# Kernel optimization log

Measured on AMD Instinct MI355X. Metric: run time of the kernel, lower is better.

Reference implementation:

```python
import jax, jax.numpy as jnp
import numpy as np

B, S, DIM, H, DH, DEPTH, NCLS = 4, 2048, 128, 8, 128, 2, 10
M = 128          # number of FAVOR+ random features
CHUNK = 128      # chunk size for causal linear attention
INNER = H * DH   # performer-pytorch: dim_head=dim -> inner_dim = heads*dim
FF = 4 * DIM


def layernorm(x, g, b, eps=1e-5):
    mu = jnp.mean(x, axis=-1, keepdims=True)
    var = jnp.mean((x - mu) ** 2, axis=-1, keepdims=True)
    return (x - mu) * jax.lax.rsqrt(var + eps) * g + b


def softmax_kernel(data, proj, is_query, eps=1e-4):
    # FAVOR+ positive softmax-kernel features. data: [B,H,S,DH], proj: [M,DH]
    norm = DH ** -0.25
    ratio = M ** -0.5
    d = data * norm
    dd = jnp.einsum('bhsd,md->bhsm', d, proj)
    diag = 0.5 * jnp.sum(d * d, axis=-1, keepdims=True)
    if is_query:
        stab = jnp.max(dd, axis=-1, keepdims=True)
    else:
        stab = jnp.max(dd, axis=(-2, -1), keepdims=True)
    stab = jax.lax.stop_gradient(stab)
    return ratio * (jnp.exp(dd - diag - stab) + eps)


def causal_linear_attention(qp, kp, v):
    # qp,kp: [B,H,S,M], v: [B,H,S,DH]; chunked prefix-sum causal linear attention
    b, h, s, m = qp.shape
    d = v.shape[-1]
    nc = s // CHUNK
    def to_chunks(t):
        return t.reshape(b, h, nc, CHUNK, -1).transpose(2, 0, 1, 3, 4)
    qc, kc, vc = to_chunks(qp), to_chunks(kp), to_chunks(v)
    tri = jnp.tril(jnp.ones((CHUNK, CHUNK), qp.dtype))
    def step(carry, inp):
        kv_sum, k_sum = carry           # [b,h,m,d], [b,h,m]
        qi, ki, vi = inp                # [b,h,CHUNK,*]
        attn = jnp.einsum('bhim,bhjm->bhij', qi, ki) * tri
        num = jnp.einsum('bhij,bhjd->bhid', attn, vi) \
            + jnp.einsum('bhim,bhmd->bhid', qi, kv_sum)
        den = jnp.sum(attn, axis=-1) + jnp.einsum('bhim,bhm->bhi', qi, k_sum)
        out = num / (den[..., None] + 1e-6)
        kv_sum = kv_sum + jnp.einsum('bhjm,bhjd->bhmd', ki, vi)
        k_sum = k_sum + jnp.sum(ki, axis=2)
        return (kv_sum, k_sum), out
    init = (jnp.zeros((b, h, m, d), qp.dtype), jnp.zeros((b, h, m), qp.dtype))
    _, out = jax.lax.scan(step, init, (qc, kc, vc))
    return out.transpose(1, 2, 0, 3, 4).reshape(b, h, s, d)


def setup_inputs():
    key = jax.random.key(0)
    ks = jax.random.split(key, 12)
    rng = np.random.default_rng(0)
    # sinusoidal positional encoding [S, DIM]
    pe = np.zeros((S, DIM), np.float32)
    pos = np.arange(S)[:, None].astype(np.float32)
    div = np.exp(np.arange(0, DIM, 2).astype(np.float32) * (-np.log(10000.0) / DIM))
    pe[:, 0::2] = np.sin(pos * div)
    pe[:, 1::2] = np.cos(pos * div)
    # orthogonal random feature projections per layer [DEPTH, M, DH]
    proj = np.stack([
        (np.linalg.qr(rng.standard_normal((DH, DH)))[0][:M] * np.sqrt(DH))
        for _ in range(DEPTH)
    ]).astype(np.float32)
    def gn(k, shape, scale):
        return jax.random.normal(k, shape, jnp.float32) * scale
    return {
        'x': gn(ks[0], (B, S, 1), 1.0),
        'lin_w': gn(ks[1], (1, DIM), 1.0),
        'lin_b': jnp.zeros((DIM,), jnp.float32),
        'pe': jnp.asarray(pe),
        'proj': jnp.asarray(proj),
        'ln1_g': jnp.ones((DEPTH, DIM), jnp.float32),
        'ln1_b': jnp.zeros((DEPTH, DIM), jnp.float32),
        'wq': gn(ks[2], (DEPTH, DIM, INNER), DIM ** -0.5),
        'wk': gn(ks[3], (DEPTH, DIM, INNER), DIM ** -0.5),
        'wv': gn(ks[4], (DEPTH, DIM, INNER), DIM ** -0.5),
        'wo': gn(ks[5], (DEPTH, INNER, DIM), INNER ** -0.5),
        'wo_b': jnp.zeros((DEPTH, DIM), jnp.float32),
        'ln2_g': jnp.ones((DEPTH, DIM), jnp.float32),
        'ln2_b': jnp.zeros((DEPTH, DIM), jnp.float32),
        'ff1_w': gn(ks[6], (DEPTH, DIM, FF), DIM ** -0.5),
        'ff1_b': jnp.zeros((DEPTH, FF), jnp.float32),
        'ff2_w': gn(ks[7], (DEPTH, FF, DIM), FF ** -0.5),
        'ff2_b': jnp.zeros((DEPTH, DIM), jnp.float32),
        'fin_w': gn(ks[8], (DIM, NCLS), DIM ** -0.5),
        'fin_b': jnp.zeros((NCLS,), jnp.float32),
    }


def reference(x, lin_w, lin_b, pe, proj, ln1_g, ln1_b, wq, wk, wv, wo, wo_b,
              ln2_g, ln2_b, ff1_w, ff1_b, ff2_w, ff2_b, fin_w, fin_b):
    h = x @ lin_w + lin_b            # [B,S,DIM]
    h = h + pe[None]
    for l in range(DEPTH):
        # --- pre-norm FAVOR+ causal self-attention ---
        y = layernorm(h, ln1_g[l], ln1_b[l])
        def split(t):  # [B,S,INNER] -> [B,H,S,DH]
            return t.reshape(B, S, H, DH).transpose(0, 2, 1, 3)
        q, k, v = split(y @ wq[l]), split(y @ wk[l]), split(y @ wv[l])
        qp = softmax_kernel(q, proj[l], True)
        kp = softmax_kernel(k, proj[l], False)
        o = causal_linear_attention(qp, kp, v)          # [B,H,S,DH]
        o = o.transpose(0, 2, 1, 3).reshape(B, S, INNER)
        h = h + (o @ wo[l] + wo_b[l])
        # --- pre-norm FFN ---
        y = layernorm(h, ln2_g[l], ln2_b[l])
        f = jax.nn.gelu(y @ ff1_w[l] + ff1_b[l]) @ ff2_w[l] + ff2_b[l]
        h = h + f
    pooled = jnp.mean(h, axis=1)     # [B,DIM]
    return pooled @ fin_w + fin_b    # [B,NCLS]
```

## Files before the change

kernel.cpp:

```cpp
#include <hip/hip_runtime.h>
#include <hip/hip_bf16.h>

#define Bb 4
#define Ss 2048
#define DIMc 128
#define Hh 8
#define DHc 128
#define Mf 128
#define CH 128
#define NCc 16
#define INNERc 1024
#define FFc 512

union F4 { float4 v; float f[4]; };
typedef unsigned short u16;

typedef __bf16 bf16x8 __attribute__((ext_vector_type(8)));
typedef float  f32x4  __attribute__((ext_vector_type(4)));

__device__ __forceinline__ unsigned fkey(float f){
  unsigned b = __float_as_uint(f);
  return (b & 0x80000000u) ? ~b : (b | 0x80000000u);
}
__device__ __forceinline__ float funkey(unsigned u){
  unsigned b = (u & 0x80000000u) ? (u & 0x7fffffffu) : ~u;
  return __uint_as_float(b);
}
__device__ __forceinline__ float gelu_f(float x){
  return 0.5f*x*(1.0f + tanhf(0.7978845608028654f*(x + 0.044715f*x*x*x)));
}
__device__ __forceinline__ u16 f2bu(float f){
  unsigned u = __float_as_uint(f);
  return (u16)((u + 0x7fffu + ((u>>16)&1u)) >> 16);
}
__device__ __forceinline__ float b2f(u16 u){
  return __uint_as_float(((unsigned)u)<<16);
}

__device__ __forceinline__ bf16x8 ldfrag(const u16* base, int row, int e){
  int byte = (row*256 + e*2) ^ ((row&7)<<4);
  return *(const bf16x8*)((const char*)base + byte);
}
__device__ __forceinline__ void stage_lin_bf(u16* dst, const u16* src, int srs, int t){
  #pragma unroll
  for(int it=0; it<8; ++it){
    int idx = t + it*256; int r = idx>>4, c8 = idx&15;
    int byte = (r*256 + c8*16) ^ ((r&7)<<4);
    *(uint4*)((char*)dst + byte) = *(const uint4*)(src + r*srs + c8*8);
  }
}
__device__ __forceinline__ void stage_lin_bf_s(u16* dst, const u16* src, int srs,
    int t, float sc, float off){
  #pragma unroll
  for(int it=0; it<8; ++it){
    int idx = t + it*256; int r = idx>>4, c8 = idx&15;
    u16 tmp[8]; *(uint4*)tmp = *(const uint4*)(src + r*srs + c8*8);
    #pragma unroll
    for(int u=0;u<8;u++) tmp[u] = f2bu(fmaf(b2f(tmp[u]), sc, off));
    int byte = (r*256 + c8*16) ^ ((r&7)<<4);
    *(uint4*)((char*)dst + byte) = *(uint4*)tmp;
  }
}
__device__ __forceinline__ void stage_lin_f32(u16* dst, const float* src, int srs, int t){
  #pragma unroll
  for(int it=0; it<8; ++it){
    int idx = t + it*256; int r = idx>>4, c8 = idx&15;
    F4 v0, v1;
    v0.v = *(const float4*)(src + r*srs + c8*8);
    v1.v = *(const float4*)(src + r*srs + c8*8 + 4);
    u16 tmp[8];
    #pragma unroll
    for(int u=0;u<4;u++){ tmp[u] = f2bu(v0.f[u]); tmp[4+u] = f2bu(v1.f[u]); }
    int byte = (r*256 + c8*16) ^ ((r&7)<<4);
    *(uint4*)((char*)dst + byte) = *(uint4*)tmp;
  }
}
__device__ __forceinline__ void stage_tr_bf(u16* dst, const u16* src, int srs, int t){
  int j0 = (t & 63)*2; int wv = t>>6;
  #pragma unroll
  for(int it=0; it<2; ++it){
    int d0 = wv*16 + it*64;
    u16 a0[16], a1[16];
    *(uint4*)&a0[0] = *(const uint4*)(src + j0*srs + d0);
    *(uint4*)&a0[8] = *(const uint4*)(src + j0*srs + d0 + 8);
    *(uint4*)&a1[0] = *(const uint4*)(src + (j0+1)*srs + d0);
    *(uint4*)&a1[8] = *(const uint4*)(src + (j0+1)*srs + d0 + 8);
    #pragma unroll
    for(int dc=0; dc<16; ++dc){
      int d = d0 + dc;
      unsigned pk = (unsigned)a0[dc] | ((unsigned)a1[dc]<<16);
      int byte = (d*256 + j0*2) ^ ((d&7)<<4);
      *(unsigned*)((char*)dst + byte) = pk;
    }
  }
}
__device__ __forceinline__ void stage_tr_bf_s(u16* dst, const u16* src, int srs,
    int t, float sc, float off){
  int j0 = (t & 63)*2; int wv = t>>6;
  #pragma unroll
  for(int it=0; it<2; ++it){
    int d0 = wv*16 + it*64;
    u16 a0[16], a1[16];
    *(uint4*)&a0[0] = *(const uint4*)(src + j0*srs + d0);
    *(uint4*)&a0[8] = *(const uint4*)(src + j0*srs + d0 + 8);
    *(uint4*)&a1[0] = *(const uint4*)(src + (j0+1)*srs + d0);
    *(uint4*)&a1[8] = *(const uint4*)(src + (j0+1)*srs + d0 + 8);
    #pragma unroll
    for(int dc=0; dc<16; ++dc){
      int d = d0 + dc;
      unsigned pk = (unsigned)f2bu(fmaf(b2f(a0[dc]), sc, off)) |
                    ((unsigned)f2bu(fmaf(b2f(a1[dc]), sc, off))<<16);
      int byte = (d*256 + j0*2) ^ ((d&7)<<4);
      *(unsigned*)((char*)dst + byte) = pk;
    }
  }
}

__device__ __forceinline__ int2 swz_tile(){
  int nx = gridDim.x;
  int nwg = gridDim.x*gridDim.y;
  int lin = blockIdx.y*nx + blockIdx.x;
  int q = nwg>>3, r = nwg&7;
  int xcd = lin&7, idx = lin>>3;
  int nl = (xcd<r) ? (xcd*(q+1)+idx) : (r*(q+1)+(xcd-r)*q+idx);
  return make_int2(nl % nx, nl / nx);
}

__global__ __launch_bounds__(256) void k_embed(const float* __restrict__ x,
    const float* __restrict__ lw, const float* __restrict__ lb,
    const float* __restrict__ pe, float* __restrict__ h,
    unsigned* __restrict__ kstab){
  if(blockIdx.x==0 && threadIdx.x<64) kstab[threadIdx.x] = 0u;
  int idx = blockIdx.x*256 + threadIdx.x;
  int d = idx & 127; int bs = idx >> 7; int s = bs & (Ss-1);
  h[idx] = x[bs]*lw[d] + lb[d] + pe[s*DIMc + d];
}

__global__ __launch_bounds__(256) void k_prep(const float* __restrict__ wo,
    const float* __restrict__ ff2, u16* __restrict__ woT, u16* __restrict__ ff2T){
  int blk = blockIdx.x;
  if(blk < 1024){
    int idx = blk*256 + threadIdx.x;
    int k = idx & 1023; int n = (idx>>10) & 127; int l = idx>>17;
    woT[idx] = f2bu(wo[l*131072 + k*128 + n]);
  } else {
    int idx = (blk-1024)*256 + threadIdx.x;
    int k = idx & 511; int n = (idx>>9) & 127; int l = idx>>16;
    ff2T[idx] = f2bu(ff2[l*65536 + k*128 + n]);
  }
}

__global__ __launch_bounds__(256) void k_ln(const float* __restrict__ in,
    const float* __restrict__ g, const float* __restrict__ bta,
    u16* __restrict__ out){
  int wave = threadIdx.x >> 6; int lane = threadIdx.x & 63;
  int row = blockIdx.x*4 + wave;
  const float* r = in + row*DIMc;
  float x1 = r[lane], x2 = r[lane+64];
  float s = x1+x2, sq = x1*x1 + x2*x2;
  #pragma unroll
  for(int m=1;m<64;m<<=1){ s += __shfl_xor(s,m,64); sq += __shfl_xor(sq,m,64); }
  float mu = s * (1.0f/128.0f);
  float var = sq*(1.0f/128.0f) - mu*mu;
  float rs = rsqrtf(var + 1e-5f);
  out[row*DIMc+lane]    = f2bu((x1-mu)*rs*g[lane]+bta[lane]);
  out[row*DIMc+lane+64] = f2bu((x2-mu)*rs*g[lane+64]+bta[lane+64]);
}

template<bool QKV3, bool BIAS, bool GELU>
__global__ __launch_bounds__(256) void k_gemm128(const u16* __restrict__ A,
    const float* __restrict__ B0, const float* __restrict__ B1,
    const float* __restrict__ B2, const float* __restrict__ bias,
    u16* __restrict__ C0, u16* __restrict__ C1, u16* __restrict__ C2,
    int N){
  __shared__ __align__(16) u16 As[16384];
  __shared__ __align__(16) u16 Bs[16384];
  int2 tt = swz_tile();
  int tn = tt.x, m0 = tt.y*128;
  const float* Bw; u16* C; int n0;
  if(QKV3){
    int tpw = N>>7;
    int widx = tn / tpw; n0 = (tn % tpw)*128;
    Bw = (widx==0) ? B0 : ((widx==1) ? B1 : B2);
    C  = (widx==0) ? C0 : ((widx==1) ? C1 : C2);
  } else { Bw = B0; C = C0; n0 = tn*128; }
  int t = threadIdx.x; int lane = t&63, w = t>>6;
  int fr = lane&15, kc = lane>>4;
  stage_lin_bf(As, A + (size_t)m0*128, 128, t);
  {
    #pragma unroll
    for(int it=0; it<8; ++it){
      int idx = t + it*256; int n = idx&127, c8 = idx>>7;
      u16 tmp[8];
      #pragma unroll
      for(int j=0;j<8;j++) tmp[j] = f2bu(Bw[(c8*8+j)*N + n0 + n]);
      int byte = (n*256 + c8*16) ^ ((n&7)<<4);
      *(uint4*)((char*)Bs + byte) = *(uint4*)tmp;
    }
  }
  __syncthreads();
  f32x4 acc[2][8] = {};
  #pragma unroll
  for(int ks=0; ks<4; ++ks){
    bf16x8 a[2];
    #pragma unroll
    for(int i=0;i<2;i++) a[i] = ldfrag(As, w*32+i*16+fr, ks*32+kc*8);
    bf16x8 bm[8];
    #pragma unroll
    for(int cb=0;cb<8;cb++) bm[cb] = ldfrag(Bs, cb*16+fr, ks*32+kc*8);
    #pragma unroll
    for(int i=0;i<2;i++)
      #pragma unroll
      for(int cb=0;cb<8;cb++)
        acc[i][cb] = __builtin_amdgcn_mfma_f32_16x16x32_bf16(a[i], bm[cb], acc[i][cb], 0,0,0);
  }
  #pragma unroll
  for(int i=0;i<2;i++){
    #pragma unroll
    for(int r=0;r<4;r++){
      int row = m0 + w*32 + i*16 + kc*4 + r;
      #pragma unroll
      for(int cb=0;cb<8;cb++){
        int col = n0 + cb*16 + fr;
        float val = acc[i][cb][r];
        if(BIAS) val += bias[col];
        if(GELU) val = gelu_f(val);
        C[(size_t)row*N + col] = f2bu(val);
      }
    }
  }
}

__global__ __launch_bounds__(256) void k_gemm_direct(const u16* __restrict__ A,
    const u16* __restrict__ BT, const float* __restrict__ bias,
    float* __restrict__ C, int N, int K){
  int2 tt = swz_tile();
  int n0 = tt.x*64, m0 = tt.y*64;
  int t = threadIdx.x; int wid = t>>6, lane = t&63;
  int wr = wid>>1, wc = wid&1;
  int fr = lane&15, kc = lane>>4;
  const u16* a0p = A  + (size_t)(m0+wr*32+fr)*K    + kc*8;
  const u16* a1p = A  + (size_t)(m0+wr*32+16+fr)*K + kc*8;
  const u16* b0p = BT + (size_t)(n0+wc*32+fr)*K    + kc*8;
  const u16* b1p = BT + (size_t)(n0+wc*32+16+fr)*K + kc*8;
  f32x4 acc[2][2] = {};
  #pragma unroll 4
  for(int k0=0; k0<K; k0+=32){
    bf16x8 af0 = *(const bf16x8*)(a0p + k0);
    bf16x8 af1 = *(const bf16x8*)(a1p + k0);
    bf16x8 bf0 = *(const bf16x8*)(b0p + k0);
    bf16x8 bf1 = *(const bf16x8*)(b1p + k0);
    acc[0][0] = __builtin_amdgcn_mfma_f32_16x16x32_bf16(af0, bf0, acc[0][0], 0,0,0);
    acc[0][1] = __builtin_amdgcn_mfma_f32_16x16x32_bf16(af0, bf1, acc[0][1], 0,0,0);
    acc[1][0] = __builtin_amdgcn_mfma_f32_16x16x32_bf16(af1, bf0, acc[1][0], 0,0,0);
    acc[1][1] = __builtin_amdgcn_mfma_f32_16x16x32_bf16(af1, bf1, acc[1][1], 0,0,0);
  }
  #pragma unroll
  for(int i=0;i<2;i++){
    #pragma unroll
    for(int r=0;r<4;r++){
      int row = m0 + wr*32 + i*16 + kc*4 + r;
      #pragma unroll
      for(int j=0;j<2;j++){
        int col = n0 + wc*32 + j*16 + fr;
        float val = acc[i][j][r] + bias[col];
        C[(size_t)row*N+col] += val;
      }
    }
  }
}

__global__ __launch_bounds__(256) void k_featboth(
    u16* __restrict__ qbuf, u16* __restrict__ kbuf,
    const float* __restrict__ proj, unsigned* __restrict__ kstab){
  __shared__ __align__(16) u16 xs[16384];
  __shared__ __align__(16) u16 ps[16384];
  __shared__ float diag_s[128];
  __shared__ unsigned hmax[8];
  int blk = blockIdx.x;
  bool isq = blk < 512;
  int r0 = (blk & 511)*128;
  u16* xin = isq ? qbuf : kbuf;
  int t = threadIdx.x; int lane = t&63, w = t>>6;
  int fr = lane&15, kc = lane>>4;
  const float norm  = 0.29730177875068026f;
  const float ratio = 0.08838834764831845f;
  if(!isq && t<8) hmax[t] = 0u;
  stage_lin_bf(xs, xin + (size_t)r0*128, 128, t);
  stage_lin_f32(ps, proj, 128, t);
  {
    int r = t>>1, half = t&1;
    const u16* rp = xin + (size_t)(r0+r)*128 + half*64;
    float ss = 0.f;
    #pragma unroll
    for(int u4=0; u4<8; ++u4){
      u16 tmp[8]; *(uint4*)tmp = *(const uint4*)(rp + u4*8);
      #pragma unroll
      for(int u=0;u<8;u++){ float f = b2f(tmp[u]); ss += f*f; }
    }
    ss += __shfl_xor(ss, 1, 64);
    if(half==0) diag_s[r] = 0.5f*norm*norm*ss;
  }
  __syncthreads();
  f32x4 acc[2][8] = {};
  #pragma unroll
  for(int ks=0; ks<4; ++ks){
    bf16x8 a[2];
    #pragma unroll
    for(int i=0;i<2;i++) a[i] = ldfrag(xs, w*32+i*16+fr, ks*32+kc*8);
    bf16x8 bm[8];
    #pragma unroll
    for(int cb=0;cb<8;cb++) bm[cb] = ldfrag(ps, cb*16+fr, ks*32+kc*8);
    #pragma unroll
    for(int i=0;i<2;i++)
      #pragma unroll
      for(int cb=0;cb<8;cb++)
        acc[i][cb] = __builtin_amdgcn_mfma_f32_16x16x32_bf16(a[i], bm[cb], acc[i][cb], 0,0,0);
  }
  __syncthreads();
  #pragma unroll
  for(int i=0;i<2;i++){
    #pragma unroll
    for(int r=0;r<4;r++){
      int row = w*32 + i*16 + kc*4 + r;
      float dg = diag_s[row];
      float rmax = acc[i][0][r];
      #pragma unroll
      for(int cb=1;cb<8;cb++) rmax = fmaxf(rmax, acc[i][cb][r]);
      #pragma unroll
      for(int msk=1;msk<16;msk<<=1) rmax = fmaxf(rmax, __shfl_xor(rmax, msk, 64));
      if(isq){
        float base = -dg - norm*rmax;
        #pragma unroll
        for(int cb=0;cb<8;cb++){
          float val = ratio*(expf(fmaf(norm, acc[i][cb][r], base)) + 1e-4f);
          int byte = (row*256 + (cb*16+fr)*2) ^ ((row&7)<<4);
          *(u16*)((char*)xs + byte) = f2bu(val);
        }
      } else {
        if(fr==0) atomicMax(&hmax[row&7], fkey(norm*rmax));
        #pragma unroll
        for(int cb=0;cb<8;cb++){
          float val = expf(fmaf(norm, acc[i][cb][r], -dg));
          int byte = (row*256 + (cb*16+fr)*2) ^ ((row&7)<<4);
          *(u16*)((char*)xs + byte) = f2bu(val);
        }
      }
    }
  }
  __syncthreads();
  #pragma unroll
  for(int it=0; it<8; ++it){
    int idx = t + it*256; int r = idx>>4, c8 = idx&15;
    int byte = (r*256 + c8*16) ^ ((r&7)<<4);
    *(uint4*)(xin + (size_t)(r0+r)*128 + c8*8) = *(uint4*)((char*)xs + byte);
  }
  if(!isq){
    int b = r0 >> 14;
    if(t<8) atomicMax(&kstab[b*8 + t], hmax[t]);
  }
}

__global__ __launch_bounds__(256) void k_attn1m(const u16* __restrict__ kp,
    const u16* __restrict__ v, u16* __restrict__ kvc, float* __restrict__ ksc,
    const unsigned* __restrict__ kstab){
  __shared__ __align__(16) u16 kt[16384];
  __shared__ __align__(16) u16 vt[16384];
  int bc = blockIdx.x; int c = bc&15, bh = bc>>4, b = bh>>3, hh = bh&7;
  int t = threadIdx.x; int lane = t&63, w = t>>6;
  int fr = lane&15, kc = lane>>4;
  int s0 = c*128;
  const float ratio = 0.08838834764831845f;
  float stab = funkey(kstab[bh]);
  float csc = ratio * expf(-stab);
  float reps = ratio * 1e-4f;
  const u16* kb = kp + (size_t)((b*Ss+s0)*Hh + hh)*128;
  const u16* vb = v  + (size_t)((b*Ss+s0)*Hh + hh)*128;
  stage_tr_bf_s(kt, kb, 1024, t, csc, reps);
  stage_tr_bf(vt, vb, 1024, t);
  __syncthreads();
  f32x4 acc[2][8] = {};
  f32x4 ks[2] = {};
  bf16x8 bones;
  #pragma unroll
  for(int e=0;e<8;e++) bones[e] = (fr==0) ? (__bf16)1.0f : (__bf16)0.0f;
  #pragma unroll
  for(int js=0;js<4;js++){
    bf16x8 am[2];
    #pragma unroll
    for(int i=0;i<2;i++) am[i] = ldfrag(kt, w*32+i*16+fr, js*32+kc*8);
    bf16x8 bv[8];
    #pragma unroll
    for(int cb=0;cb<8;cb++) bv[cb] = ldfrag(vt, cb*16+fr, js*32+kc*8);
    #pragma unroll
    for(int i=0;i<2;i++){
      ks[i] = __builtin_amdgcn_mfma_f32_16x16x32_bf16(am[i], bones, ks[i], 0,0,0);
      #pragma unroll
      for(int cb=0;cb<8;cb++)
        acc[i][cb] = __builtin_amdgcn_mfma_f32_16x16x32_bf16(am[i], bv[cb], acc[i][cb], 0,0,0);
    }
  }
  u16* kvb = kvc + (size_t)bc*16384;
  #pragma unroll
  for(int i=0;i<2;i++){
    #pragma unroll
    for(int r=0;r<4;r++){
      int m = w*32 + i*16 + kc*4 + r;
      #pragma unroll
      for(int cb=0;cb<8;cb++) kvb[m*128 + cb*16 + fr] = f2bu(acc[i][cb][r]);
      if(fr==0) ksc[bc*128 + m] = ks[i][r];
    }
  }
}

__global__ __launch_bounds__(256) void k_prefix2(unsigned* __restrict__ kvc,
    float* __restrict__ ksc){
  int blk = blockIdx.x;
  if(blk < 1024){
    int bh = blk >> 5; int pos = (blk & 31)*256 + threadIdx.x;
    int base = bh*16*8192 + pos;
    float a0 = 0.f, a1 = 0.f;
    #pragma unroll
    for(int c=0;c<16;c++){
      unsigned pk = kvc[base + c*8192];
      float x0 = b2f((u16)pk), x1 = b2f((u16)(pk>>16));
      kvc[base + c*8192] = (unsigned)f2bu(a0) | ((unsigned)f2bu(a1)<<16);
      a0 += x0; a1 += x1;
    }
  } else {
    int e = (blk-1024)*256 + threadIdx.x;
    int bh = e>>7, m = e&127;
    float a = 0.f;
    #pragma unroll
    for(int c=0;c<16;c++){
      int idx = (bh*16+c)*128 + m;
      float xv = ksc[idx]; ksc[idx] = a; a += xv;
    }
  }
}

__global__ __launch_bounds__(256) void k_attn2m(const u16* __restrict__ qp,
    const u16* __restrict__ kp, const u16* __restrict__ v,
    const u16* __restrict__ kvc, const float* __restrict__ ksc,
    u16* __restrict__ o, const unsigned* __restrict__ kstab){
  __shared__ __align__(16) u16 qs[16384];
  __shared__ __align__(16) u16 bs[16384];
  __shared__ float ksum_s[128];
  int bc = blockIdx.x; int c = bc&15, bh = bc>>4, b = bh>>3, hh = bh&7;
  int t = threadIdx.x; int lane = t&63, w = t>>6;
  int fr = lane&15, kc = lane>>4;
  int s0 = c*128;
  const float ratio = 0.08838834764831845f;
  float stab = funkey(kstab[bh]);
  float csc = ratio * expf(-stab);
  float reps = ratio * 1e-4f;
  const u16* qb = qp + (size_t)((b*Ss+s0)*Hh + hh)*128;
  const u16* kb = kp + (size_t)((b*Ss+s0)*Hh + hh)*128;
  const u16* vb = v  + (size_t)((b*Ss+s0)*Hh + hh)*128;
  const u16* kvb = kvc + (size_t)bc*16384;
  stage_lin_bf(qs, qb, 1024, t);
  stage_lin_bf_s(bs, kb, 1024, t, csc, reps);
  if(t<128) ksum_s[t] = ksc[bc*128 + t];
  __syncthreads();
  bf16x8 aq[2][4];
  #pragma unroll
  for(int i=0;i<2;i++)
    #pragma unroll
    for(int ks=0;ks<4;ks++)
      aq[i][ks] = ldfrag(qs, w*32+i*16+fr, ks*32+kc*8);
  f32x4 sacc[2][8] = {};
  #pragma unroll
  for(int ks=0;ks<4;ks++){
    bf16x8 bk[8];
    #pragma unroll
    for(int cb=0;cb<8;cb++) bk[cb] = ldfrag(bs, cb*16+fr, ks*32+kc*8);
    #pragma unroll
    for(int i=0;i<2;i++)
      #pragma unroll
      for(int cb=0;cb<8;cb++)
        sacc[i][cb] = __builtin_amdgcn_mfma_f32_16x16x32_bf16(aq[i][ks], bk[cb], sacc[i][cb], 0,0,0);
  }
  __syncthreads();
  #pragma unroll
  for(int i=0;i<2;i++){
    #pragma unroll
    for(int cb=0;cb<8;cb++){
      #pragma unroll
      for(int r=0;r<4;r++){
        int prow = w*32 + i*16 + kc*4 + r;
        int pcol = cb*16 + fr;
        float pv = (pcol > prow) ? 0.f : sacc[i][cb][r];
        int byte = (prow*256 + pcol*2) ^ ((prow&7)<<4);
        *(u16*)((char*)qs + byte) = f2bu(pv);
      }
    }
  }
  stage_tr_bf(bs, vb, 1024, t);
  __syncthreads();
  f32x4 nacc[2][8] = {};
  f32x4 dacc[2] = {};
  bf16x8 bones;
  #pragma unroll
  for(int e=0;e<8;e++) bones[e] = (fr==0) ? (__bf16)1.0f : (__bf16)0.0f;
  #pragma unroll
  for(int js=0;js<4;js++){
    bf16x8 ap[2];
    #pragma unroll
    for(int i=0;i<2;i++) ap[i] = ldfrag(qs, w*32+i*16+fr, js*32+kc*8);
    bf16x8 bv[8];
    #pragma unroll
    for(int cb=0;cb<8;cb++) bv[cb] = ldfrag(bs, cb*16+fr, js*32+kc*8);
    #pragma unroll
    for(int i=0;i<2;i++){
      dacc[i] = __builtin_amdgcn_mfma_f32_16x16x32_bf16(ap[i], bones, dacc[i], 0,0,0);
      #pragma unroll
      for(int cb=0;cb<8;cb++)
        nacc[i][cb] = __builtin_amdgcn_mfma_f32_16x16x32_bf16(ap[i], bv[cb], nacc[i][cb], 0,0,0);
    }
  }
  __syncthreads();
  stage_tr_bf(bs, kvb, 128, t);
  __syncthreads();
  #pragma unroll
  for(int ms=0;ms<4;ms++){
    bf16x8 bkv[8];
    #pragma unroll
    for(int cb=0;cb<8;cb++) bkv[cb] = ldfrag(bs, cb*16+fr, ms*32+kc*8);
    bf16x8 bks;
    #pragma unroll
    for(int e=0;e<8;e++) bks[e] = (fr==0) ? (__bf16)ksum_s[ms*32+kc*8+e] : (__bf16)0.0f;
    #pragma unroll
    for(int i=0;i<2;i++){
      dacc[i] = __builtin_amdgcn_mfma_f32_16x16x32_bf16(aq[i][ms], bks, dacc[i], 0,0,0);
      #pragma unroll
      for(int cb=0;cb<8;cb++)
        nacc[i][cb] = __builtin_amdgcn_mfma_f32_16x16x32_bf16(aq[i][ms], bkv[cb], nacc[i][cb], 0,0,0);
    }
  }
  #pragma unroll
  for(int i=0;i<2;i++){
    #pragma unroll
    for(int r=0;r<4;r++){
      float den = __shfl(dacc[i][r], lane & 48, 64);
      float inv = 1.0f/(den + 1e-6f);
      int row = w*32 + i*16 + kc*4 + r;
      u16* ob = o + (size_t)((b*Ss+s0+row)*Hh + hh)*128;
      #pragma unroll
      for(int cb=0;cb<8;cb++)
        ob[cb*16 + fr] = f2bu(nacc[i][cb][r] * inv);
    }
  }
}

__global__ __launch_bounds__(256) void k_pool(const float* __restrict__ h,
    float* __restrict__ pw){
  __shared__ float part[256];
  int blk = blockIdx.x; int b = blk>>4, c = blk&15;
  int t = threadIdx.x; int half = t>>7;
  float s = 0.f;
  int s0 = c*128 + half*64;
  for(int si=s0; si<s0+64; ++si) s += h[(b*Ss+si)*128 + (t&127)];
  part[t] = s;
  __syncthreads();
  if(t<128) pw[blk*128 + t] = part[t] + part[t+128];
}
__global__ __launch_bounds__(128) void k_cls(const float* __restrict__ pw,
    const float* __restrict__ fw, const float* __restrict__ fb,
    float* __restrict__ out){
  __shared__ float pool_s[128];
  int b = blockIdx.x; int t = threadIdx.x;
  float s = 0.f;
  for(int c=0;c<16;c++) s += pw[(b*16+c)*128 + t];
  pool_s[t] = s * (1.0f/2048.0f);
  __syncthreads();
  if(t<10){
    float a = fb[t];
    for(int d=0; d<128; ++d) a += pool_s[d]*fw[d*10+t];
    out[b*10+t] = a;
  }
}

extern "C" void kernel_launch(void* const* d_in, const int* in_sizes, int n_in,
                              void* d_out, int out_size, void* d_ws, size_t ws_size,
                              hipStream_t stream){
  (void)in_sizes; (void)n_in; (void)out_size; (void)ws_size;
  const float* x     = (const float*)d_in[0];
  const float* lin_w = (const float*)d_in[1];
  const float* lin_b = (const float*)d_in[2];
  const float* pe    = (const float*)d_in[3];
  const float* proj  = (const float*)d_in[4];
  const float* ln1_g = (const float*)d_in[5];
  const float* ln1_b = (const float*)d_in[6];
  const float* wq    = (const float*)d_in[7];
  const float* wk    = (const float*)d_in[8];
  const float* wv    = (const float*)d_in[9];
  const float* wo    = (const float*)d_in[10];
  const float* wo_b  = (const float*)d_in[11];
  const float* ln2_g = (const float*)d_in[12];
  const float* ln2_b = (const float*)d_in[13];
  const float* ff1w  = (const float*)d_in[14];
  const float* ff1b  = (const float*)d_in[15];
  const float* ff2w  = (const float*)d_in[16];
  const float* ff2b  = (const float*)d_in[17];
  const float* finw  = (const float*)d_in[18];
  const float* finb  = (const float*)d_in[19];
  float* out = (float*)d_out;

  float* ws  = (float*)d_ws;
  float* h    = ws;
  u16*  y    = (u16*)(h + 1048576);
  u16*  q    = (u16*)(h + 1048576 + 524288);
  u16*  k    = q + 8388608;
  u16*  v    = k + 8388608;
  u16*  o    = v + 8388608;
  u16*  kvc  = o + 8388608;
  float* ksc  = (float*)(kvc + 8388608);
  float* pw   = ksc + 65536;
  unsigned* kstab = (unsigned*)(pw + 8192);
  u16*  woT  = (u16*)(kstab + 64);
  u16*  ff2T = woT + 262144;

  k_embed<<<4096,256,0,stream>>>(x, lin_w, lin_b, pe, h, kstab);
  k_prep<<<1536,256,0,stream>>>(wo, ff2w, woT, ff2T);
  for(int l=0;l<2;l++){
    const float* projl = proj + l*Mf*DHc;
    k_ln<<<2048,256,0,stream>>>(h, ln1_g + l*DIMc, ln1_b + l*DIMc, y);
    k_gemm128<true,false,false><<<dim3(24,64),256,0,stream>>>(
        y, wq + l*DIMc*INNERc, wk + l*DIMc*INNERc, wv + l*DIMc*INNERc,
        nullptr, q, k, v, INNERc);
    k_featboth<<<1024,256,0,stream>>>(q, k, projl, kstab + l*32);
    k_attn1m<<<512,256,0,stream>>>(k, v, kvc, ksc, kstab + l*32);
    k_prefix2<<<1040,256,0,stream>>>((unsigned*)kvc, ksc);
    k_attn2m<<<512,256,0,stream>>>(q, k, v, kvc, ksc, o, kstab + l*32);
    k_gemm_direct<<<dim3(2,128),256,0,stream>>>(o, woT + l*131072, wo_b + l*DIMc, h, DIMc, INNERc);
    k_ln<<<2048,256,0,stream>>>(h, ln2_g + l*DIMc, ln2_b + l*DIMc, y);
    k_gemm128<false,true,true><<<dim3(4,64),256,0,stream>>>(
        y, ff1w + l*DIMc*FFc, nullptr, nullptr, ff1b + l*FFc,
        q, nullptr, nullptr, FFc);
    k_gemm_direct<<<dim3(2,128),256,0,stream>>>(q, ff2T + l*65536, ff2b + l*DIMc, h, DIMc, FFc);
  }
  k_pool<<<64,256,0,stream>>>(h, pw);
  k_cls<<<4,128,0,stream>>>(pw, finw, finb, out);
}
```

Measured before the change: 408.5 us.

## Fuse LayerNorm into embedding and residual GEMM epilogues

Removes the standalone LayerNorm kernels. LN1 of layer 0 is folded into the embedding kernel, and each following LayerNorm is computed in the epilogue of the residual-add GEMM (out-proj and FF2). To do that, the residual GEMM is reshaped so each block owns 32 full rows across all 128 columns, with row statistics reduced via shuffles and shared memory. This saves launches and a full re-read of h per LayerNorm. In exchange the GEMM grid drops to 256 blocks, each doing more MFMA work per wave, which may reduce parallelism.

```diff
diff --git a/kernel.cpp b/kernel.cpp
--- a/kernel.cpp
+++ b/kernel.cpp
@@ -125,15 +125,35 @@
   int nl = (xcd<r) ? (xcd*(q+1)+idx) : (r*(q+1)+(xcd-r)*q+idx);
   return make_int2(nl % nx, nl / nx);
 }
-
-__global__ __launch_bounds__(256) void k_embed(const float* __restrict__ x,
+__device__ __forceinline__ int swz_lin(){
+  int nwg = gridDim.x;
+  int lin = blockIdx.x;
+  int q = nwg>>3;
+  return (lin&7)*q + (lin>>3);
+}
+
+__global__ __launch_bounds__(256) void k_embed_ln(const float* __restrict__ x,
     const float* __restrict__ lw, const float* __restrict__ lb,
-    const float* __restrict__ pe, float* __restrict__ h,
-    unsigned* __restrict__ kstab){
+    const float* __restrict__ pe, const float* __restrict__ g,
+    const float* __restrict__ bta, float* __restrict__ h,
+    u16* __restrict__ y, unsigned* __restrict__ kstab){
   if(blockIdx.x==0 && threadIdx.x<64) kstab[threadIdx.x] = 0u;
-  int idx = blockIdx.x*256 + threadIdx.x;
-  int d = idx & 127; int bs = idx >> 7; int s = bs & (Ss-1);
-  h[idx] = x[bs]*lw[d] + lb[d] + pe[s*DIMc + d];
+  int wave = threadIdx.x >> 6; int lane = threadIdx.x & 63;
+  int row = blockIdx.x*4 + wave;
+  int s = row & (Ss-1);
+  float xv = x[row];
+  float x1 = xv*lw[lane]    + lb[lane]    + pe[s*DIMc + lane];
+  float x2 = xv*lw[lane+64] + lb[lane+64] + pe[s*DIMc + lane+64];
+  h[row*DIMc+lane]    = x1;
+  h[row*DIMc+lane+64] = x2;
+  float sm = x1+x2, sq = x1*x1 + x2*x2;
+  #pragma unroll
+  for(int m=1;m<64;m<<=1){ sm += __shfl_xor(sm,m,64); sq += __shfl_xor(sq,m,64); }
+  float mu = sm * (1.0f/128.0f);
+  float var = sq*(1.0f/128.0f) - mu*mu;
+  float rs = rsqrtf(var + 1e-5f);
+  y[row*DIMc+lane]    = f2bu((x1-mu)*rs*g[lane]+bta[lane]);
+  y[row*DIMc+lane+64] = f2bu((x2-mu)*rs*g[lane+64]+bta[lane+64]);
 }
 
 __global__ __launch_bounds__(256) void k_prep(const float* __restrict__ wo,
@@ -148,23 +168,6 @@
     int k = idx & 511; int n = (idx>>9) & 127; int l = idx>>16;
     ff2T[idx] = f2bu(ff2[l*65536 + k*128 + n]);
   }
-}
-
-__global__ __launch_bounds__(256) void k_ln(const float* __restrict__ in,
-    const float* __restrict__ g, const float* __restrict__ bta,
-    u16* __restrict__ out){
-  int wave = threadIdx.x >> 6; int lane = threadIdx.x & 63;
-  int row = blockIdx.x*4 + wave;
-  const float* r = in + row*DIMc;
-  float x1 = r[lane], x2 = r[lane+64];
-  float s = x1+x2, sq = x1*x1 + x2*x2;
-  #pragma unroll
-  for(int m=1;m<64;m<<=1){ s += __shfl_xor(s,m,64); sq += __shfl_xor(sq,m,64); }
-  float mu = s * (1.0f/128.0f);
-  float var = sq*(1.0f/128.0f) - mu*mu;
-  float rs = rsqrtf(var + 1e-5f);
-  out[row*DIMc+lane]    = f2bu((x1-mu)*rs*g[lane]+bta[lane]);
-  out[row*DIMc+lane+64] = f2bu((x2-mu)*rs*g[lane+64]+bta[lane+64]);
 }
 
 template<bool QKV3, bool BIAS, bool GELU>
@@ -231,40 +234,64 @@
   }
 }
 
-__global__ __launch_bounds__(256) void k_gemm_direct(const u16* __restrict__ A,
+template<bool DOLN>
+__global__ __launch_bounds__(256) void k_gemm_direct_ln(const u16* __restrict__ A,
     const u16* __restrict__ BT, const float* __restrict__ bias,
-    float* __restrict__ C, int N, int K){
-  int2 tt = swz_tile();
-  int n0 = tt.x*64, m0 = tt.y*64;
-  int t = threadIdx.x; int wid = t>>6, lane = t&63;
-  int wr = wid>>1, wc = wid&1;
+    float* __restrict__ h, const float* __restrict__ g,
+    const float* __restrict__ bta, u16* __restrict__ y, int K){
+  __shared__ float sums_s[32][2], sqs_s[32][2];
+  int m0 = swz_lin()*32;
+  int t = threadIdx.x; int w = t>>6, lane = t&63;
+  int rg = w>>1, ch = w&1;
   int fr = lane&15, kc = lane>>4;
-  const u16* a0p = A  + (size_t)(m0+wr*32+fr)*K    + kc*8;
-  const u16* a1p = A  + (size_t)(m0+wr*32+16+fr)*K + kc*8;
-  const u16* b0p = BT + (size_t)(n0+wc*32+fr)*K    + kc*8;
-  const u16* b1p = BT + (size_t)(n0+wc*32+16+fr)*K + kc*8;
-  f32x4 acc[2][2] = {};
+  const u16* ap = A + (size_t)(m0+rg*16+fr)*K + kc*8;
+  const u16* bp[4];
+  #pragma unroll
+  for(int cb=0;cb<4;cb++) bp[cb] = BT + (size_t)(ch*64+cb*16+fr)*K + kc*8;
+  f32x4 acc[4] = {};
   #pragma unroll 4
   for(int k0=0; k0<K; k0+=32){
-    bf16x8 af0 = *(const bf16x8*)(a0p + k0);
-    bf16x8 af1 = *(const bf16x8*)(a1p + k0);
-    bf16x8 bf0 = *(const bf16x8*)(b0p + k0);
-    bf16x8 bf1 = *(const bf16x8*)(b1p + k0);
-    acc[0][0] = __builtin_amdgcn_mfma_f32_16x16x32_bf16(af0, bf0, acc[0][0], 0,0,0);
-    acc[0][1] = __builtin_amdgcn_mfma_f32_16x16x32_bf16(af0, bf1, acc[0][1], 0,0,0);
-    acc[1][0] = __builtin_amdgcn_mfma_f32_16x16x32_bf16(af1, bf0, acc[1][0], 0,0,0);
-    acc[1][1] = __builtin_amdgcn_mfma_f32_16x16x32_bf16(af1, bf1, acc[1][1], 0,0,0);
-  }
-  #pragma unroll
-  for(int i=0;i<2;i++){
+    bf16x8 af = *(const bf16x8*)(ap + k0);
+    #pragma unroll
+    for(int cb=0;cb<4;cb++){
+      bf16x8 bf = *(const bf16x8*)(bp[cb] + k0);
+      acc[cb] = __builtin_amdgcn_mfma_f32_16x16x32_bf16(af, bf, acc[cb], 0,0,0);
+    }
+  }
+  float hv[4][4];
+  #pragma unroll
+  for(int r=0;r<4;r++){
+    int row = m0 + rg*16 + kc*4 + r;
+    float s = 0.f, sq = 0.f;
+    #pragma unroll
+    for(int cb=0;cb<4;cb++){
+      int col = ch*64 + cb*16 + fr;
+      float val = acc[cb][r] + bias[col] + h[(size_t)row*128+col];
+      h[(size_t)row*128+col] = val;
+      hv[r][cb] = val;
+      if(DOLN){ s += val; sq += val*val; }
+    }
+    if(DOLN){
+      #pragma unroll
+      for(int msk=1;msk<16;msk<<=1){ s += __shfl_xor(s,msk,64); sq += __shfl_xor(sq,msk,64); }
+      if(fr==0){ sums_s[rg*16+kc*4+r][ch] = s; sqs_s[rg*16+kc*4+r][ch] = sq; }
+    }
+  }
+  if(DOLN){
+    __syncthreads();
     #pragma unroll
     for(int r=0;r<4;r++){
-      int row = m0 + wr*32 + i*16 + kc*4 + r;
-      #pragma unroll
-      for(int j=0;j<2;j++){
-        int col = n0 + wc*32 + j*16 + fr;
-        float val = acc[i][j][r] + bias[col];
-        C[(size_t)row*N+col] += val;
+      int rw = rg*16 + kc*4 + r;
+      int row = m0 + rw;
+      float s  = sums_s[rw][0] + sums_s[rw][1];
+      float sq = sqs_s[rw][0] + sqs_s[rw][1];
+      float mu = s * (1.0f/128.0f);
+      float var = sq*(1.0f/128.0f) - mu*mu;
+      float rs = rsqrtf(var + 1e-5f);
+      #pragma unroll
+      for(int cb=0;cb<4;cb++){
+        int col = ch*64 + cb*16 + fr;
+        y[(size_t)row*128+col] = f2bu((hv[r][cb]-mu)*rs*g[col] + bta[col]);
       }
     }
   }
@@ -620,11 +647,10 @@
   u16*  woT  = (u16*)(kstab + 64);
   u16*  ff2T = woT + 262144;
 
-  k_embed<<<4096,256,0,stream>>>(x, lin_w, lin_b, pe, h, kstab);
+  k_embed_ln<<<2048,256,0,stream>>>(x, lin_w, lin_b, pe, ln1_g, ln1_b, h, y, kstab);
   k_prep<<<1536,256,0,stream>>>(wo, ff2w, woT, ff2T);
   for(int l=0;l<2;l++){
     const float* projl = proj + l*Mf*DHc;
-    k_ln<<<2048,256,0,stream>>>(h, ln1_g + l*DIMc, ln1_b + l*DIMc, y);
     k_gemm128<true,false,false><<<dim3(24,64),256,0,stream>>>(
         y, wq + l*DIMc*INNERc, wk + l*DIMc*INNERc, wv + l*DIMc*INNERc,
         nullptr, q, k, v, INNERc);
@@ -632,12 +658,17 @@
     k_attn1m<<<512,256,0,stream>>>(k, v, kvc, ksc, kstab + l*32);
     k_prefix2<<<1040,256,0,stream>>>((unsigned*)kvc, ksc);
     k_attn2m<<<512,256,0,stream>>>(q, k, v, kvc, ksc, o, kstab + l*32);
-    k_gemm_direct<<<dim3(2,128),256,0,stream>>>(o, woT + l*131072, wo_b + l*DIMc, h, DIMc, INNERc);
-    k_ln<<<2048,256,0,stream>>>(h, ln2_g + l*DIMc, ln2_b + l*DIMc, y);
+    k_gemm_direct_ln<true><<<256,256,0,stream>>>(o, woT + l*131072,
+        wo_b + l*DIMc, h, ln2_g + l*DIMc, ln2_b + l*DIMc, y, INNERc);
     k_gemm128<false,true,true><<<dim3(4,64),256,0,stream>>>(
         y, ff1w + l*DIMc*FFc, nullptr, nullptr, ff1b + l*FFc,
         q, nullptr, nullptr, FFc);
-    k_gemm_direct<<<dim3(2,128),256,0,stream>>>(q, ff2T + l*65536, ff2b + l*DIMc, h, DIMc, FFc);
+    if(l==0)
+      k_gemm_direct_ln<true><<<256,256,0,stream>>>(q, ff2T + l*65536,
+          ff2b + l*DIMc, h, ln1_g + (l+1)*DIMc, ln1_b + (l+1)*DIMc, y, FFc);
+    else
+      k_gemm_direct_ln<false><<<256,256,0,stream>>>(q, ff2T + l*65536,
+          ff2b + l*DIMc, h, nullptr, nullptr, nullptr, FFc);
   }
   k_pool<<<64,256,0,stream>>>(h, pw);
   k_cls<<<4,128,0,stream>>>(pw, finw, finb, out);
```

Measured after the change: 439.7 us. +7.6%, slower.

## Pre-transpose all weights to bf16 once and fuse embedding with first layernorm

Applied to the files above, without the earlier changes.

A single tiled prep kernel now converts wq/wk/wv/ff1 (as well as wo/ff2) to transposed bf16 through shared memory with vectorized loads and stores. The GEMM then stages B with the same linear bf16 loader used for A, replacing per-tile strided fp32 gathers and conversions. The embedding kernel also computes the first layernorm, which removes one launch and one pass over h. The cost is a larger workspace and a prep kernel with only 80 blocks.

```diff
diff --git a/kernel.cpp b/kernel.cpp
--- a/kernel.cpp
+++ b/kernel.cpp
@@ -126,28 +126,28 @@
   return make_int2(nl % nx, nl / nx);
 }
 
-__global__ __launch_bounds__(256) void k_embed(const float* __restrict__ x,
+__global__ __launch_bounds__(256) void k_embed_ln(const float* __restrict__ x,
     const float* __restrict__ lw, const float* __restrict__ lb,
-    const float* __restrict__ pe, float* __restrict__ h,
-    unsigned* __restrict__ kstab){
+    const float* __restrict__ pe, const float* __restrict__ g,
+    const float* __restrict__ bta, float* __restrict__ h,
+    u16* __restrict__ y, unsigned* __restrict__ kstab){
   if(blockIdx.x==0 && threadIdx.x<64) kstab[threadIdx.x] = 0u;
-  int idx = blockIdx.x*256 + threadIdx.x;
-  int d = idx & 127; int bs = idx >> 7; int s = bs & (Ss-1);
-  h[idx] = x[bs]*lw[d] + lb[d] + pe[s*DIMc + d];
-}
-
-__global__ __launch_bounds__(256) void k_prep(const float* __restrict__ wo,
-    const float* __restrict__ ff2, u16* __restrict__ woT, u16* __restrict__ ff2T){
-  int blk = blockIdx.x;
-  if(blk < 1024){
-    int idx = blk*256 + threadIdx.x;
-    int k = idx & 1023; int n = (idx>>10) & 127; int l = idx>>17;
-    woT[idx] = f2bu(wo[l*131072 + k*128 + n]);
-  } else {
-    int idx = (blk-1024)*256 + threadIdx.x;
-    int k = idx & 511; int n = (idx>>9) & 127; int l = idx>>16;
-    ff2T[idx] = f2bu(ff2[l*65536 + k*128 + n]);
-  }
+  int wave = threadIdx.x >> 6; int lane = threadIdx.x & 63;
+  int row = blockIdx.x*4 + wave;
+  int s = row & (Ss-1);
+  float xv = x[row];
+  float x1 = xv*lw[lane]    + lb[lane]    + pe[s*DIMc + lane];
+  float x2 = xv*lw[lane+64] + lb[lane+64] + pe[s*DIMc + lane+64];
+  h[row*DIMc+lane]    = x1;
+  h[row*DIMc+lane+64] = x2;
+  float sm = x1+x2, sq = x1*x1 + x2*x2;
+  #pragma unroll
+  for(int m=1;m<64;m<<=1){ sm += __shfl_xor(sm,m,64); sq += __shfl_xor(sq,m,64); }
+  float mu = sm * (1.0f/128.0f);
+  float var = sq*(1.0f/128.0f) - mu*mu;
+  float rs = rsqrtf(var + 1e-5f);
+  y[row*DIMc+lane]    = f2bu((x1-mu)*rs*g[lane]+bta[lane]);
+  y[row*DIMc+lane+64] = f2bu((x2-mu)*rs*g[lane+64]+bta[lane+64]);
 }
 
 __global__ __launch_bounds__(256) void k_ln(const float* __restrict__ in,
@@ -167,37 +167,66 @@
   out[row*DIMc+lane+64] = f2bu((x2-mu)*rs*g[lane+64]+bta[lane+64]);
 }
 
+__global__ __launch_bounds__(256) void k_prep(const float* __restrict__ wq,
+    const float* __restrict__ wk, const float* __restrict__ wv,
+    const float* __restrict__ ff1, const float* __restrict__ wo,
+    const float* __restrict__ ff2, u16* __restrict__ qkvT,
+    u16* __restrict__ ff1T, u16* __restrict__ woT, u16* __restrict__ ff2T){
+  __shared__ u16 tile[128][136];
+  int blk = blockIdx.x, t = threadIdx.x;
+  const float* src; u16* dst; int srcN, dstK, k0, n0;
+  if(blk < 48){
+    int l = blk/24, m = (blk%24)>>3, nt = blk&7;
+    const float* W = (m==0) ? wq : ((m==1) ? wk : wv);
+    src = W + l*131072; srcN = 1024; k0 = 0; n0 = nt*128;
+    dst = qkvT + ((size_t)(l*3+m)*1024 + n0)*128; dstK = 128;
+  } else if(blk < 64){
+    int i = blk-48; int l = i>>3, kt = i&7;
+    src = wo + l*131072; srcN = 128; k0 = kt*128; n0 = 0;
+    dst = woT + (size_t)l*131072; dstK = 1024;
+  } else if(blk < 72){
+    int i = blk-64; int l = i>>2, nt = i&3;
+    src = ff1 + l*65536; srcN = 512; k0 = 0; n0 = nt*128;
+    dst = ff1T + ((size_t)l*512 + n0)*128; dstK = 128;
+  } else {
+    int i = blk-72; int l = i>>2, kt = i&3;
+    src = ff2 + l*65536; srcN = 128; k0 = kt*128; n0 = 0;
+    dst = ff2T + (size_t)l*65536; dstK = 512;
+  }
+  #pragma unroll
+  for(int it=0; it<16; ++it){
+    int idx = t + it*256; int kk = idx>>5, n4 = idx&31;
+    F4 v; v.v = *(const float4*)(src + (size_t)(k0+kk)*srcN + n0 + n4*4);
+    #pragma unroll
+    for(int j=0;j<4;j++) tile[n4*4+j][kk] = f2bu(v.f[j]);
+  }
+  __syncthreads();
+  #pragma unroll
+  for(int it=0; it<8; ++it){
+    int idx = t + it*256; int n = idx>>4, kq = idx&15;
+    *(uint4*)(dst + (size_t)n*dstK + k0 + kq*8) = *(uint4*)&tile[n][kq*8];
+  }
+}
+
 template<bool QKV3, bool BIAS, bool GELU>
 __global__ __launch_bounds__(256) void k_gemm128(const u16* __restrict__ A,
-    const float* __restrict__ B0, const float* __restrict__ B1,
-    const float* __restrict__ B2, const float* __restrict__ bias,
+    const u16* __restrict__ BT, const float* __restrict__ bias,
     u16* __restrict__ C0, u16* __restrict__ C1, u16* __restrict__ C2,
     int N){
   __shared__ __align__(16) u16 As[16384];
   __shared__ __align__(16) u16 Bs[16384];
   int2 tt = swz_tile();
   int tn = tt.x, m0 = tt.y*128;
-  const float* Bw; u16* C; int n0;
+  const u16* Bbase; u16* C; int n0;
   if(QKV3){
-    int tpw = N>>7;
-    int widx = tn / tpw; n0 = (tn % tpw)*128;
-    Bw = (widx==0) ? B0 : ((widx==1) ? B1 : B2);
-    C  = (widx==0) ? C0 : ((widx==1) ? C1 : C2);
-  } else { Bw = B0; C = C0; n0 = tn*128; }
+    int widx = tn>>3; n0 = (tn&7)*128;
+    Bbase = BT + (size_t)widx*131072 + (size_t)n0*128;
+    C = (widx==0) ? C0 : ((widx==1) ? C1 : C2);
+  } else { n0 = tn*128; Bbase = BT + (size_t)n0*128; C = C0; }
   int t = threadIdx.x; int lane = t&63, w = t>>6;
   int fr = lane&15, kc = lane>>4;
   stage_lin_bf(As, A + (size_t)m0*128, 128, t);
-  {
-    #pragma unroll
-    for(int it=0; it<8; ++it){
-      int idx = t + it*256; int n = idx&127, c8 = idx>>7;
-      u16 tmp[8];
-      #pragma unroll
-      for(int j=0;j<8;j++) tmp[j] = f2bu(Bw[(c8*8+j)*N + n0 + n]);
-      int byte = (n*256 + c8*16) ^ ((n&7)<<4);
-      *(uint4*)((char*)Bs + byte) = *(uint4*)tmp;
-    }
-  }
+  stage_lin_bf(Bs, Bbase, 128, t);
   __syncthreads();
   f32x4 acc[2][8] = {};
   #pragma unroll
@@ -619,15 +648,16 @@
   unsigned* kstab = (unsigned*)(pw + 8192);
   u16*  woT  = (u16*)(kstab + 64);
   u16*  ff2T = woT + 262144;
-
-  k_embed<<<4096,256,0,stream>>>(x, lin_w, lin_b, pe, h, kstab);
-  k_prep<<<1536,256,0,stream>>>(wo, ff2w, woT, ff2T);
+  u16*  qkvT = ff2T + 131072;
+  u16*  ff1T = qkvT + 786432;
+
+  k_embed_ln<<<2048,256,0,stream>>>(x, lin_w, lin_b, pe, ln1_g, ln1_b, h, y, kstab);
+  k_prep<<<80,256,0,stream>>>(wq, wk, wv, ff1w, wo, ff2w, qkvT, ff1T, woT, ff2T);
   for(int l=0;l<2;l++){
     const float* projl = proj + l*Mf*DHc;
-    k_ln<<<2048,256,0,stream>>>(h, ln1_g + l*DIMc, ln1_b + l*DIMc, y);
+    if(l) k_ln<<<2048,256,0,stream>>>(h, ln1_g + l*DIMc, ln1_b + l*DIMc, y);
     k_gemm128<true,false,false><<<dim3(24,64),256,0,stream>>>(
-        y, wq + l*DIMc*INNERc, wk + l*DIMc*INNERc, wv + l*DIMc*INNERc,
-        nullptr, q, k, v, INNERc);
+        y, qkvT + (size_t)l*393216, nullptr, q, k, v, INNERc);
     k_featboth<<<1024,256,0,stream>>>(q, k, projl, kstab + l*32);
     k_attn1m<<<512,256,0,stream>>>(k, v, kvc, ksc, kstab + l*32);
     k_prefix2<<<1040,256,0,stream>>>((unsigned*)kvc, ksc);
@@ -635,8 +665,7 @@
     k_gemm_direct<<<dim3(2,128),256,0,stream>>>(o, woT + l*131072, wo_b + l*DIMc, h, DIMc, INNERc);
     k_ln<<<2048,256,0,stream>>>(h, ln2_g + l*DIMc, ln2_b + l*DIMc, y);
     k_gemm128<false,true,true><<<dim3(4,64),256,0,stream>>>(
-        y, ff1w + l*DIMc*FFc, nullptr, nullptr, ff1b + l*FFc,
-        q, nullptr, nullptr, FFc);
+        y, ff1T + (size_t)l*65536, ff1b + l*FFc, q, nullptr, nullptr, FFc);
     k_gemm_direct<<<dim3(2,128),256,0,stream>>>(q, ff2T + l*65536, ff2b + l*DIMc, h, DIMc, FFc);
   }
   k_pool<<<64,256,0,stream>>>(h, pw);
```

Measured after the change: 400.6 us. No clear change (-1.9%).
